# Optimization experiments

Hardware: AMD Instinct MI355X
Metric: run time of the kernel (lower is better)

The kernel has to match this reference:

```python
import jax, jax.numpy as jnp
import numpy as np

N0, N1, N2 = 200_000, 100_000, 80_000
F = 32
K5, K3 = 125, 27
M1, M2, M3, M4 = 20_000, 20_000, 30_000, 20_000
EPS = 1e-5


def sparse_conv(feats, W, in_idx, out_idx, n_out):
    """Gather-GEMM-scatter sparse conv. feats:[Nin,Cin], W:[K,Cin,Cout],
    in_idx/out_idx:[K,M] kernel map. Returns [n_out, Cout]."""
    g = feats[in_idx]                                  # [K, M, Cin] gather
    contrib = jnp.einsum('kmc,kcd->kmd', g, W)         # per-offset GEMM
    cout = W.shape[-1]
    out = jnp.zeros((n_out, cout), feats.dtype)
    return out.at[out_idx.reshape(-1)].add(contrib.reshape(-1, cout))


def bn(x, g, b):
    m = x.mean(0)
    v = x.var(0)
    return (x - m) * jax.lax.rsqrt(v + EPS) * g + b


def setup_inputs():
    key = jax.random.key(0)
    ks = jax.random.split(key, 16)
    W_SCALE = 0.02
    inp = {
        'x_feats': jax.random.normal(ks[0], (N0, 1), jnp.float32),
        'w1a': jax.random.normal(ks[1], (K5, 1, F), jnp.float32) * W_SCALE,
        'w1b': jax.random.normal(ks[2], (K5, F, F), jnp.float32) * W_SCALE,
        'w1c': jax.random.normal(ks[3], (K5, F, F), jnp.float32) * W_SCALE,
        'w2': jax.random.normal(ks[4], (K3, F, 2 * F), jnp.float32) * W_SCALE,
        'w3a': jax.random.normal(ks[5], (K3, 2 * F, 4 * F), jnp.float32) * W_SCALE,
        'w3b': jax.random.normal(ks[6], (K3, 4 * F, 8 * F), jnp.float32) * W_SCALE,
        'bn1b_g': jnp.ones((F,), jnp.float32), 'bn1b_b': jnp.zeros((F,), jnp.float32),
        'bn1c_g': jnp.ones((F,), jnp.float32), 'bn1c_b': jnp.zeros((F,), jnp.float32),
        'bn3a_g': jnp.ones((4 * F,), jnp.float32), 'bn3a_b': jnp.zeros((4 * F,), jnp.float32),
        'bn3b_g': jnp.ones((8 * F,), jnp.float32), 'bn3b_b': jnp.zeros((8 * F,), jnp.float32),
        'km1a_in': jax.random.randint(ks[7], (K5, M1), 0, N0, jnp.int32),
        'km1a_out': jax.random.randint(ks[8], (K5, M1), 0, N1, jnp.int32),
        'km1b_in': jax.random.randint(ks[9], (K5, M2), 0, N1, jnp.int32),
        'km1b_out': jax.random.randint(ks[10], (K5, M2), 0, N1, jnp.int32),
        'km1c_in': jax.random.randint(ks[11], (K5, M2), 0, N1, jnp.int32),
        'km1c_out': jax.random.randint(ks[12], (K5, M2), 0, N1, jnp.int32),
        'km2_in': jax.random.randint(ks[13], (K3, M3), 0, N1, jnp.int32),
        'km2_out': jax.random.randint(ks[14], (K3, M3), 0, N2, jnp.int32),
        'km3a_in': jax.random.randint(jax.random.fold_in(key, 20), (K3, M4), 0, N2, jnp.int32),
        'km3a_out': jax.random.randint(jax.random.fold_in(key, 21), (K3, M4), 0, N2, jnp.int32),
        'km3b_in': jax.random.randint(jax.random.fold_in(key, 22), (K3, M4), 0, N2, jnp.int32),
        'km3b_out': jax.random.randint(jax.random.fold_in(key, 23), (K3, M4), 0, N2, jnp.int32),
        'n1': N1,
        'n2': N2,
    }
    return inp


def reference(x_feats, w1a, w1b, w1c, w2, w3a, w3b,
              bn1b_g, bn1b_b, bn1c_g, bn1c_b, bn3a_g, bn3a_b, bn3b_g, bn3b_b,
              km1a_in, km1a_out, km1b_in, km1b_out, km1c_in, km1c_out,
              km2_in, km2_out, km3a_in, km3a_out, km3b_in, km3b_out, n1, n2):
    # enc1: conv(1->F, k5, s2) + ReLU
    h = jax.nn.relu(sparse_conv(x_feats, w1a, km1a_in, km1a_out, n1))
    # conv(F->F, k5) + BN + ReLU
    h = jax.nn.relu(bn(sparse_conv(h, w1b, km1b_in, km1b_out, n1), bn1b_g, bn1b_b))
    # conv(F->F, k5) + BN + ReLU
    x_e1 = jax.nn.relu(bn(sparse_conv(h, w1c, km1c_in, km1c_out, n1), bn1c_g, bn1c_b))
    # conv2: conv(F->2F, k3) onto c_out coordinates (no activation)
    h2 = sparse_conv(x_e1, w2, km2_in, km2_out, n2)
    # enc2: conv(2F->4F, k3) + BN + ReLU
    h2 = jax.nn.relu(bn(sparse_conv(h2, w3a, km3a_in, km3a_out, n2), bn3a_g, bn3a_b))
    # conv(4F->8F, k3) + BN + ReLU
    x_e2 = jax.nn.relu(bn(sparse_conv(h2, w3b, km3b_in, km3b_out, n2), bn3b_g, bn3b_b))
    return (x_e1, x_e2)
```

## Files before the change

kernel.cpp:

```cpp
#include <hip/hip_runtime.h>
#include <hip/hip_fp16.h>
#include <cstdint>
#include <algorithm>

#define N1c 100000
#define N2c 80000
#define EPSc 1e-5f
#define STRIDE_N1 102400
#define STRIDE_N2 81920

typedef _Float16 fp16x8 __attribute__((ext_vector_type(8)));
typedef float f32x4 __attribute__((ext_vector_type(4)));

__global__ __launch_bounds__(256) void rank2d_kernel(
    const int* __restrict__ out_idx, int* __restrict__ rank,
    int* __restrict__ bins, int E, int M, int q, int stride)
{
    for (int e = blockIdx.x * 256 + threadIdx.x; e < E; e += gridDim.x * 256) {
        int chunk = (e / M) / q;
        rank[e] = atomicAdd(&bins[chunk * stride + out_idx[e]], 1);
    }
}

__global__ __launch_bounds__(256) void scan1(
    const int* __restrict__ bins, int* __restrict__ ptr,
    int* __restrict__ bsums, int n)
{
    __shared__ int lds[256];
    int base = blockIdx.x * 1024;
    int v[4]; int t = 0;
    #pragma unroll
    for (int i = 0; i < 4; ++i) {
        int idx = base + threadIdx.x * 4 + i;
        v[i] = idx < n ? bins[idx] : 0;
        t += v[i];
    }
    lds[threadIdx.x] = t; __syncthreads();
    for (int off = 1; off < 256; off <<= 1) {
        int x = threadIdx.x >= off ? lds[threadIdx.x - off] : 0;
        __syncthreads();
        lds[threadIdx.x] += x;
        __syncthreads();
    }
    int run = lds[threadIdx.x] - t;
    if (threadIdx.x == 255) bsums[blockIdx.x] = lds[255];
    #pragma unroll
    for (int i = 0; i < 4; ++i) {
        int idx = base + threadIdx.x * 4 + i;
        if (idx < n) ptr[idx] = run;
        run += v[i];
    }
}

__global__ __launch_bounds__(64) void scan2s(
    int* __restrict__ bsums, int bpc, int nch)
{
    int c = threadIdx.x;
    if (c < nch) {
        int run = 0;
        for (int i = 0; i < bpc; ++i) {
            int idx = c * bpc + i;
            int t = bsums[idx]; bsums[idx] = run; run += t;
        }
    }
}

__global__ __launch_bounds__(256) void scan3(
    int* __restrict__ ptr, const int* __restrict__ bsums, int n)
{
    int idx = blockIdx.x * 1024 + threadIdx.x * 4;
    int add = bsums[blockIdx.x];
    #pragma unroll
    for (int i = 0; i < 4; ++i)
        if (idx + i < n) ptr[idx + i] += add;
}

__global__ __launch_bounds__(256) void wconv_fp16(
    const float* __restrict__ W, _Float16* __restrict__ Wh,
    int K, int CIN, int CTILE, int WST, int total)
{
    for (int idx = blockIdx.x * 256 + threadIdx.x; idx < total;
         idx += gridDim.x * 256) {
        int k = idx / (CTILE * CIN);
        int c = (idx / CIN) % CTILE;
        int j = idx % CIN;
        Wh[idx] = (_Float16)W[(size_t)k * CIN * WST + (size_t)j * WST + c];
    }
}

__global__ __launch_bounds__(256) void scatter_1a(
    const float* __restrict__ x, const int* __restrict__ iin,
    const int* __restrict__ iout, const int* __restrict__ ptr,
    const int* __restrict__ rank, float2* __restrict__ payload, int E, int M)
{
    for (int e = blockIdx.x * 256 + threadIdx.x; e < E; e += gridDim.x * 256) {
        int k = e / M;
        float2 p; p.x = x[iin[e]]; p.y = __int_as_float(k);
        payload[ptr[iout[e]] + rank[e]] = p;
    }
}

__global__ __launch_bounds__(256) void phaseB_1a(
    const float2* __restrict__ payload, const int* __restrict__ ptr,
    const float* __restrict__ W, __half* __restrict__ out, int n)
{
    __shared__ float Wl[125 * 32];
    for (int i = threadIdx.x; i < 125 * 32; i += 256) Wl[i] = W[i];
    __syncthreads();
    int total = n * 32;
    for (int idx = blockIdx.x * 256 + threadIdx.x; idx < total; idx += gridDim.x * 256) {
        int o = idx >> 5, c = idx & 31;
        int s0 = ptr[o], s1 = ptr[o + 1];
        float acc = 0.f;
        for (int s = s0; s < s1; ++s) {
            float2 p = payload[s];
            acc = fmaf(p.x, Wl[(__float_as_int(p.y) << 5) + c], acc);
        }
        out[idx] = __float2half(fmaxf(acc, 0.f));
    }
}

template <int CIN, int CTILE, int GMODE, int IN16>
__global__ __launch_bounds__(256, 3) void phaseA_mfma(
    const void* __restrict__ feats_, const _Float16* __restrict__ Wh,
    const int* __restrict__ in_idx, const int* __restrict__ out_idx,
    const int* __restrict__ ptr, const int* __restrict__ rank,
    __half* __restrict__ contrib, int M,
    const float* __restrict__ sc, const float* __restrict__ sh)
{
    constexpr int PP  = 64;
    constexpr int NK  = CIN / 32;
    constexpr int NCF = CTILE / 16;
    constexpr int GCHK = CIN / 8;
    constexpr int GSM  = (GCHK < 16 ? GCHK : 16) - 1;
    constexpr int RCH  = GCHK / 4;
    static_assert(CIN % 32 == 0 && CTILE % 16 == 0 && RCH >= 1, "");

    __shared__ __align__(16) _Float16 Gl[PP * CIN];
    __shared__ __align__(16) _Float16 Wt[CTILE * CIN];
    __shared__ int sslot[PP];

    const int tid  = threadIdx.x;
    const int wave = tid >> 6;
    const int lane = tid & 63;
    const int k    = blockIdx.y;

    const int* iin  = in_idx  + (size_t)k * M;
    const int* iout = out_idx + (size_t)k * M;
    const int* rk   = rank    + (size_t)k * M;
    const _Float16* Wk = Wh + (size_t)k * CTILE * CIN;

    for (int i = tid; i < CTILE * GCHK; i += 256) {
        int row = i / GCHK, ch = i % GCHK;
        fp16x8 v = *(const fp16x8*)&Wk[(size_t)row * CIN + ch * 8];
        *(fp16x8*)&Wt[row * CIN + ((ch ^ (row & GSM)) << 3)] = v;
    }

    for (int base = blockIdx.x * PP; base < M; base += gridDim.x * PP) {
        if (tid < PP && base + tid < M)
            sslot[tid] = ptr[iout[base + tid]] + rk[base + tid];

        {
            int r = tid & 63;
            int h = tid >> 6;
            int p = base + r;
            if (p < M) {
                const int c0 = h * (CIN / 4);
                if (IN16) {
                    const _Float16* fr =
                        (const _Float16*)feats_ + (size_t)iin[p] * CIN + c0;
                    #pragma unroll
                    for (int cc = 0; cc < RCH; ++cc) {
                        int c = cc * 8;
                        fp16x8 v = *(const fp16x8*)(fr + c);
                        if (GMODE == 2) {
                            #pragma unroll
                            for (int j = 0; j < 8; ++j) {
                                float x = fmaf((float)v[j], sc[c0 + c + j],
                                               sh[c0 + c + j]);
                                v[j] = (_Float16)fmaxf(x, 0.f);
                            }
                        }
                        int ch = (c0 + c) >> 3;
                        *(fp16x8*)&Gl[r * CIN + ((ch ^ (r & GSM)) << 3)] = v;
                    }
                } else {
                    const float* fr =
                        (const float*)feats_ + (size_t)iin[p] * CIN + c0;
                    #pragma unroll
                    for (int cc = 0; cc < RCH; ++cc) {
                        int c = cc * 8;
                        float a[8];
                        *(float4*)&a[0] = *(const float4*)(fr + c);
                        *(float4*)&a[4] = *(const float4*)(fr + c + 4);
                        if (GMODE == 2) {
                            #pragma unroll
                            for (int j = 0; j < 8; ++j)
                                a[j] = fmaxf(fmaf(a[j], sc[c0 + c + j],
                                                  sh[c0 + c + j]), 0.f);
                        }
                        fp16x8 v;
                        #pragma unroll
                        for (int j = 0; j < 8; ++j) v[j] = (_Float16)a[j];
                        int ch = (c0 + c) >> 3;
                        *(fp16x8*)&Gl[r * CIN + ((ch ^ (r & GSM)) << 3)] = v;
                    }
                }
            }
        }
        __syncthreads();

        f32x4 acc[NCF];
        #pragma unroll
        for (int cf = 0; cf < NCF; ++cf)
            acc[cf] = (f32x4){0.f, 0.f, 0.f, 0.f};

        const int lrow = lane & 15;
        const int lk8  = (lane >> 4) * 8;
        #pragma unroll
        for (int kk = 0; kk < NK; ++kk) {
            int col = kk * 32 + lk8;
            int r = wave * 16 + lrow;
            fp16x8 afr = *(const fp16x8*)
                &Gl[r * CIN + ((((col >> 3) ^ (r & GSM))) << 3)];
            #pragma unroll
            for (int cf = 0; cf < NCF; ++cf) {
                int rw = cf * 16 + lrow;
                fp16x8 bfr = *(const fp16x8*)
                    &Wt[rw * CIN + ((((col >> 3) ^ (rw & GSM))) << 3)];
                acc[cf] = __builtin_amdgcn_mfma_f32_16x16x32_f16(
                    afr, bfr, acc[cf], 0, 0, 0);
            }
        }

        {
            int prb = wave * 16 + (lane >> 4) * 4;
            #pragma unroll
            for (int b = 0; b < 4; ++b) {
                int pr = prb + b;
                if (base + pr < M) {
                    size_t s = (size_t)sslot[pr];
                    #pragma unroll
                    for (int cf = 0; cf < NCF; ++cf)
                        contrib[s * CTILE + cf * 16 + lrow] =
                            __float2half(acc[cf][b]);
                }
            }
        }
        __syncthreads();
    }
}

template <int CSTR, bool STATS, int OUT16>
__global__ __launch_bounds__(256) void phaseB8(
    const __half* __restrict__ contrib, const int* __restrict__ ptr,
    void* __restrict__ out_, int n, int ostr, int accum,
    double* __restrict__ statsbuf, int sqoff)
{
    float s1 = 0.f, s2 = 0.f;
    int total = n * CSTR;
    for (int idx = blockIdx.x * 256 + threadIdx.x; idx < total; idx += gridDim.x * 256) {
        int o = idx / CSTR, c = idx % CSTR;
        int a = ptr[o], b = ptr[o + 1];
        size_t oi = (size_t)o * ostr + c;
        float acc;
        if (OUT16)
            acc = accum ? __half2float(((const __half*)out_)[oi]) : 0.f;
        else
            acc = accum ? ((const float*)out_)[oi] : 0.f;
        for (int s = a; s < b; ++s)
            acc += __half2float(contrib[(size_t)s * CSTR + c]);
        if (OUT16) ((__half*)out_)[oi] = __float2half(acc);
        else       ((float*)out_)[oi] = acc;
        if (STATS) { s1 += acc; s2 += acc * acc; }
    }
    if constexpr (STATS) {
        __shared__ double l1[256], l2[256];
        l1[threadIdx.x] = (double)s1; l2[threadIdx.x] = (double)s2;
        __syncthreads();
        for (int off = 128; off >= CSTR; off >>= 1) {
            if (threadIdx.x < (unsigned)off) {
                l1[threadIdx.x] += l1[threadIdx.x + off];
                l2[threadIdx.x] += l2[threadIdx.x + off];
            }
            __syncthreads();
        }
        if (threadIdx.x < CSTR) {
            atomicAdd(&statsbuf[threadIdx.x], l1[threadIdx.x]);
            atomicAdd(&statsbuf[sqoff + threadIdx.x], l2[threadIdx.x]);
        }
    }
}

template <int C>
__global__ __launch_bounds__(256) void make_scsh(
    const double* __restrict__ sums, const float* __restrict__ g,
    const float* __restrict__ b, float* __restrict__ sc, float* __restrict__ sh,
    double inv_n)
{
    int c = threadIdx.x;
    if (c < C) {
        double mean = sums[c] * inv_n;
        double var  = sums[C + c] * inv_n - mean * mean;
        float s = g[c] * (float)(1.0 / sqrt(var + (double)EPSc));
        sc[c] = s;
        sh[c] = b[c] - (float)mean * s;
    }
}

template <int C>
__global__ __launch_bounds__(256) void bn_apply_relu_kernel(
    float* __restrict__ x, int n, const double* __restrict__ sums,
    const float* __restrict__ g, const float* __restrict__ b)
{
    const int c = threadIdx.x % C;
    const double inv_n = 1.0 / (double)n;
    double mean = sums[c] * inv_n;
    double var  = sums[C + c] * inv_n - mean * mean;
    float scale = g[c] * (float)(1.0 / sqrt(var + (double)EPSc));
    float shift = b[c] - (float)mean * scale;
    size_t total = (size_t)n * C;
    size_t stride = (size_t)gridDim.x * 256;
    for (size_t i = (size_t)blockIdx.x * 256 + threadIdx.x; i < total; i += stride)
        x[i] = fmaxf(x[i] * scale + shift, 0.f);
}

struct Plan { int q, nch; };

static Plan make_plan(long long tot_elems, int K, long long cap, int maxch)
{
    if (cap < 1) cap = 1;
    long long nch0 = (tot_elems + cap - 1) / cap;
    if (nch0 < 1) nch0 = 1;
    if (nch0 > K) nch0 = K;
    int q = (int)((K + nch0 - 1) / nch0);
    int nch = (K + q - 1) / q;
    if (nch > maxch) { q = (K + maxch - 1) / maxch; nch = (K + q - 1) / q; }
    return { q, nch };
}

static void build_csr2d(const int* iout, int* rank, int* bins, int* ptr, int* bsums,
                        int E, int M, int q, int nch, int stride, hipStream_t s)
{
    hipMemsetAsync(bins, 0, (size_t)nch * stride * sizeof(int), s);
    int gb = std::min(2048, (E + 255) / 256);
    hipLaunchKernelGGL(rank2d_kernel, dim3(gb), dim3(256), 0, s, iout, rank, bins, E, M, q, stride);
    int totalbins = nch * stride, nb = totalbins / 1024, bpc = stride / 1024;
    hipLaunchKernelGGL(scan1, dim3(nb), dim3(256), 0, s, bins, ptr, bsums, totalbins);
    hipLaunchKernelGGL(scan2s, dim3(1), dim3(64), 0, s, bsums, bpc, nch);
    hipLaunchKernelGGL(scan3, dim3(nb), dim3(256), 0, s, ptr, bsums, totalbins);
}

template <int CIN, int COUT, int GMODE, bool STATS, int IN16, int OUT16>
static void run_layer(const void* feats, const float* W,
                      const int* iin, const int* iout, void* outp,
                      int M, int K, int n_out, int stride, int maxch,
                      int* bins, int* ptr, int* bsums, int* rank, __half* contrib,
                      _Float16* wh, long long cap_f32,
                      const float* sc, const float* sh,
                      double* statsbuf, hipStream_t s)
{
    int wtot = K * COUT * CIN;
    hipLaunchKernelGGL(wconv_fp16, dim3(std::min(2048, (wtot + 255) / 256)),
                       dim3(256), 0, s, W, wh, K, CIN, COUT, COUT, wtot);
    long long cap_h = cap_f32 * 2;
    Plan pl = make_plan((long long)K * M * COUT, K, cap_h, maxch);
    build_csr2d(iout, rank, bins, ptr, bsums, K * M, M, pl.q, pl.nch, stride, s);
    for (int ch = 0; ch < pl.nch; ++ch) {
        int k0 = ch * pl.q;
        int qc = std::min(pl.q, K - k0);
        dim3 g((M + 63) / 64, qc);
        hipLaunchKernelGGL((phaseA_mfma<CIN, COUT, GMODE, IN16>), g, dim3(256), 0, s,
                           feats, wh + (size_t)k0 * COUT * CIN,
                           iin + (size_t)k0 * M, iout + (size_t)k0 * M,
                           ptr + (size_t)ch * stride, rank + (size_t)k0 * M,
                           contrib, M, sc, sh);
        bool last = (ch == pl.nch - 1);
        if (STATS && last)
            hipLaunchKernelGGL((phaseB8<COUT, true, OUT16>), dim3(2048), dim3(256), 0, s,
                               contrib, ptr + (size_t)ch * stride, outp, n_out, COUT,
                               ch ? 1 : 0, statsbuf, COUT);
        else
            hipLaunchKernelGGL((phaseB8<COUT, false, OUT16>), dim3(2048), dim3(256), 0, s,
                               contrib, ptr + (size_t)ch * stride, outp, n_out, COUT,
                               ch ? 1 : 0, (double*)nullptr, 0);
    }
}

extern "C" void kernel_launch(void* const* d_in, const int* in_sizes, int n_in,
                              void* d_out, int out_size, void* d_ws, size_t ws_size,
                              hipStream_t stream)
{
    const float* x_feats = (const float*)d_in[0];
    const float* w1a = (const float*)d_in[1];
    const float* w1b = (const float*)d_in[2];
    const float* w1c = (const float*)d_in[3];
    const float* w2  = (const float*)d_in[4];
    const float* w3a = (const float*)d_in[5];
    const float* w3b = (const float*)d_in[6];
    const float* bn1b_g = (const float*)d_in[7];
    const float* bn1b_b = (const float*)d_in[8];
    const float* bn1c_g = (const float*)d_in[9];
    const float* bn1c_b = (const float*)d_in[10];
    const float* bn3a_g = (const float*)d_in[11];
    const float* bn3a_b = (const float*)d_in[12];
    const float* bn3b_g = (const float*)d_in[13];
    const float* bn3b_b = (const float*)d_in[14];
    const int* km1a_in  = (const int*)d_in[15];
    const int* km1a_out = (const int*)d_in[16];
    const int* km1b_in  = (const int*)d_in[17];
    const int* km1b_out = (const int*)d_in[18];
    const int* km1c_in  = (const int*)d_in[19];
    const int* km1c_out = (const int*)d_in[20];
    const int* km2_in   = (const int*)d_in[21];
    const int* km2_out  = (const int*)d_in[22];
    const int* km3a_in  = (const int*)d_in[23];
    const int* km3a_out = (const int*)d_in[24];
    const int* km3b_in  = (const int*)d_in[25];
    const int* km3b_out = (const int*)d_in[26];

    float* out  = (float*)d_out;
    float* x_e1 = out;
    float* x_e2 = out + (size_t)N1c * 32;

    float* ws = (float*)d_ws;
    float*  poolA  = ws;
    float*  poolB  = poolA + 10240000;
    double* dstats = (double*)(poolB + 5120000);
    float*  scsh   = (float*)(dstats + 2048);
    int*    bins   = (int*)(scsh + 1024);
    int*    ptr    = bins + 819200;
    int*    bsums  = ptr + 819200;
    int*    rank   = bsums + 1024;
    float*  whf    = (float*)(rank + 2500000);
    _Float16* wh   = (_Float16*)whf;
    float*  contribf = whf + 221200;
    __half* contrib  = (__half*)contribf;
    const long long FIXED = 10240000LL + 5120000 + 4096 + 1024
                          + 819200 + 819200 + 1024 + 2500000 + 221200;
    long long cap = (long long)(ws_size / 4) - FIXED - 32;
    if (cap < 1) cap = 1;

    __half* h1  = (__half*)poolA;
    __half* h3  = (__half*)poolA;
    __half* h2  = (__half*)poolB;
    __half* h2b = (__half*)poolB;

    double* dst1b = dstats;
    double* dst1c = dstats + 512;
    double* dst3a = dstats + 1024;
    double* dst3b = dstats + 1536;
    float* sc1b = scsh,       *sh1b = scsh + 32;
    float* sc3a = scsh + 256, *sh3a = scsh + 384;

    hipMemsetAsync(dstats, 0, 2048 * sizeof(double), stream);

    {
        build_csr2d(km1a_out, rank, bins, ptr, bsums, 125 * 20000, 20000, 125, 1,
                    STRIDE_N1, stream);
        hipLaunchKernelGGL(scatter_1a, dim3(2048), dim3(256), 0, stream,
                           x_feats, km1a_in, km1a_out, ptr, rank, (float2*)contribf,
                           125 * 20000, 20000);
        hipLaunchKernelGGL(phaseB_1a, dim3(2048), dim3(256), 0, stream,
                           (const float2*)contribf, ptr, w1a, h1, N1c);
    }

    run_layer<32, 32, 0, true, 1, 1>(h1, w1b, km1b_in, km1b_out, h2, 20000, 125, N1c,
                                     STRIDE_N1, 8, bins, ptr, bsums, rank, contrib,
                                     wh, cap, nullptr, nullptr, dst1b, stream);
    hipLaunchKernelGGL((make_scsh<32>), dim3(1), dim3(256), 0, stream,
                       dst1b, bn1b_g, bn1b_b, sc1b, sh1b, 1.0 / N1c);

    run_layer<32, 32, 2, true, 1, 0>(h2, w1c, km1c_in, km1c_out, x_e1, 20000, 125, N1c,
                                     STRIDE_N1, 8, bins, ptr, bsums, rank, contrib,
                                     wh, cap, sc1b, sh1b, dst1c, stream);
    hipLaunchKernelGGL((bn_apply_relu_kernel<32>), dim3(2048), dim3(256), 0, stream,
                       x_e1, N1c, dst1c, bn1c_g, bn1c_b);

    run_layer<32, 64, 0, false, 0, 1>(x_e1, w2, km2_in, km2_out, h2b, 30000, 27, N2c,
                                      STRIDE_N2, 10, bins, ptr, bsums, rank, contrib,
                                      wh, cap, nullptr, nullptr, nullptr, stream);

    run_layer<64, 128, 0, true, 1, 1>(h2b, w3a, km3a_in, km3a_out, h3, 20000, 27, N2c,
                                      STRIDE_N2, 10, bins, ptr, bsums, rank, contrib,
                                      wh, cap, nullptr, nullptr, dst3a, stream);
    hipLaunchKernelGGL((make_scsh<128>), dim3(1), dim3(256), 0, stream,
                       dst3a, bn3a_g, bn3a_b, sc3a, sh3a, 1.0 / N2c);

    {
        const int M = 20000, K = 27;
        Plan pl = make_plan((long long)K * M * 128, K, cap * 2, 10);
        build_csr2d(km3b_out, rank, bins, ptr, bsums, K * M, M, pl.q, pl.nch,
                    STRIDE_N2, stream);
        for (int half = 0; half < 2; ++half) {
            int wtot = K * 128 * 128;
            hipLaunchKernelGGL(wconv_fp16, dim3(2048), dim3(256), 0, stream,
                               w3b + half * 128, wh, K, 128, 128, 256, wtot);
            for (int ch = 0; ch < pl.nch; ++ch) {
                int k0 = ch * pl.q;
                int qc = std::min(pl.q, K - k0);
                dim3 g((20000 + 63) / 64, qc);
                hipLaunchKernelGGL((phaseA_mfma<128, 128, 2, 1>), g, dim3(256), 0, stream,
                                   h3, wh + (size_t)k0 * 128 * 128,
                                   km3b_in + (size_t)k0 * M, km3b_out + (size_t)k0 * M,
                                   ptr + (size_t)ch * STRIDE_N2, rank + (size_t)k0 * M,
                                   contrib, M, sc3a, sh3a);
                bool last = (ch == pl.nch - 1);
                if (last)
                    hipLaunchKernelGGL((phaseB8<128, true, 0>), dim3(2048), dim3(256), 0, stream,
                                       contrib, ptr + (size_t)ch * STRIDE_N2,
                                       x_e2 + half * 128, N2c, 256, ch ? 1 : 0,
                                       dst3b + half * 128, 256);
                else
                    hipLaunchKernelGGL((phaseB8<128, false, 0>), dim3(2048), dim3(256), 0, stream,
                                       contrib, ptr + (size_t)ch * STRIDE_N2,
                                       x_e2 + half * 128, N2c, 256, ch ? 1 : 0,
                                       (double*)nullptr, 0);
            }
        }
        hipLaunchKernelGGL((bn_apply_relu_kernel<256>), dim3(2048), dim3(256), 0, stream,
                           x_e2, N2c, dst3b, bn3b_g, bn3b_b);
    }
}
```

Measured before the change: 1.898 ms.

## Compute all 256 output channels of last conv in one pass; fp16 shadow for conv2 input

The final 128->256 sparse conv used to run twice, once per 128-channel half, which repeated the gather, the CSR chunk loop and the scatter-reduce passes. A new MFMA kernel gathers each input row once and loops over both weight halves in shared memory, writing 256-wide fp16 contributions that a single phaseB pass reduces. This removes the duplicate gather and reduction work but doubles the contribution buffer per chunk, which can mean more chunks and a larger LDS footprint. Separately, the BN-apply for x_e1 now also writes an fp16 copy, so conv2 gathers half-width features instead of fp32.

Result: faster. 1.841 ms (-3.0%).

```diff
diff --git a/kernel.cpp b/kernel.cpp
--- a/kernel.cpp
+++ b/kernel.cpp
@@ -251,6 +251,113 @@
     }
 }
 
+template <int GMODE>
+__global__ __launch_bounds__(256, 3) void phaseA_mfma_3b(
+    const void* __restrict__ feats_, const _Float16* __restrict__ Wh,
+    const int* __restrict__ in_idx, const int* __restrict__ out_idx,
+    const int* __restrict__ ptr, const int* __restrict__ rank,
+    __half* __restrict__ contrib, int M,
+    const float* __restrict__ sc, const float* __restrict__ sh)
+{
+    constexpr int CIN = 128, PP = 64, NK = 4, NCF = 8;
+    constexpr int GCHK = 16, GSM = 15, RCH = 4;
+
+    __shared__ __align__(16) _Float16 Gl[PP * CIN];
+    __shared__ __align__(16) _Float16 Wt[128 * CIN];
+    __shared__ int sslot[PP];
+
+    const int tid  = threadIdx.x;
+    const int wave = tid >> 6;
+    const int lane = tid & 63;
+    const int k    = blockIdx.y;
+
+    const _Float16* feats = (const _Float16*)feats_;
+    const int* iin  = in_idx  + (size_t)k * M;
+    const int* iout = out_idx + (size_t)k * M;
+    const int* rk   = rank    + (size_t)k * M;
+    const _Float16* Wk = Wh + (size_t)k * 256 * CIN;
+
+    const int lrow = lane & 15;
+    const int lk8  = (lane >> 4) * 8;
+
+    for (int base = blockIdx.x * PP; base < M; base += gridDim.x * PP) {
+        if (tid < PP && base + tid < M)
+            sslot[tid] = ptr[iout[base + tid]] + rk[base + tid];
+
+        {
+            int r = tid & 63;
+            int h = tid >> 6;
+            int p = base + r;
+            if (p < M) {
+                const int c0 = h * 32;
+                const _Float16* fr = feats + (size_t)iin[p] * CIN + c0;
+                #pragma unroll
+                for (int cc = 0; cc < RCH; ++cc) {
+                    int c = cc * 8;
+                    fp16x8 v = *(const fp16x8*)(fr + c);
+                    if (GMODE == 2) {
+                        #pragma unroll
+                        for (int j = 0; j < 8; ++j) {
+                            float x = fmaf((float)v[j], sc[c0 + c + j],
+                                           sh[c0 + c + j]);
+                            v[j] = (_Float16)fmaxf(x, 0.f);
+                        }
+                    }
+                    int ch = (c0 + c) >> 3;
+                    *(fp16x8*)&Gl[r * CIN + ((ch ^ (r & GSM)) << 3)] = v;
+                }
+            }
+        }
+
+        #pragma unroll
+        for (int half = 0; half < 2; ++half) {
+            __syncthreads();
+            for (int i = tid; i < 128 * GCHK; i += 256) {
+                int row = i / GCHK, ch = i % GCHK;
+                fp16x8 v = *(const fp16x8*)
+                    &Wk[(size_t)(half * 128 + row) * CIN + ch * 8];
+                *(fp16x8*)&Wt[row * CIN + ((ch ^ (row & GSM)) << 3)] = v;
+            }
+            __syncthreads();
+
+            f32x4 acc[NCF];
+            #pragma unroll
+            for (int cf = 0; cf < NCF; ++cf)
+                acc[cf] = (f32x4){0.f, 0.f, 0.f, 0.f};
+
+            #pragma unroll
+            for (int kk = 0; kk < NK; ++kk) {
+                int col = kk * 32 + lk8;
+                int r = wave * 16 + lrow;
+                fp16x8 afr = *(const fp16x8*)
+                    &Gl[r * CIN + ((((col >> 3) ^ (r & GSM))) << 3)];
+                #pragma unroll
+                for (int cf = 0; cf < NCF; ++cf) {
+                    int rw = cf * 16 + lrow;
+                    fp16x8 bfr = *(const fp16x8*)
+                        &Wt[rw * CIN + ((((col >> 3) ^ (rw & GSM))) << 3)];
+                    acc[cf] = __builtin_amdgcn_mfma_f32_16x16x32_f16(
+                        afr, bfr, acc[cf], 0, 0, 0);
+                }
+            }
+
+            int prb = wave * 16 + (lane >> 4) * 4;
+            #pragma unroll
+            for (int b = 0; b < 4; ++b) {
+                int pr = prb + b;
+                if (base + pr < M) {
+                    size_t s = (size_t)sslot[pr];
+                    #pragma unroll
+                    for (int cf = 0; cf < NCF; ++cf)
+                        contrib[s * 256 + half * 128 + cf * 16 + lrow] =
+                            __float2half(acc[cf][b]);
+                }
+            }
+        }
+        __syncthreads();
+    }
+}
+
 template <int CSTR, bool STATS, int OUT16>
 __global__ __launch_bounds__(256) void phaseB8(
     const __half* __restrict__ contrib, const int* __restrict__ ptr,
@@ -323,6 +430,27 @@
     size_t stride = (size_t)gridDim.x * 256;
     for (size_t i = (size_t)blockIdx.x * 256 + threadIdx.x; i < total; i += stride)
         x[i] = fmaxf(x[i] * scale + shift, 0.f);
+}
+
+template <int C>
+__global__ __launch_bounds__(256) void bn_apply_relu_shadow_kernel(
+    float* __restrict__ x, __half* __restrict__ xh, int n,
+    const double* __restrict__ sums,
+    const float* __restrict__ g, const float* __restrict__ b)
+{
+    const int c = threadIdx.x % C;
+    const double inv_n = 1.0 / (double)n;
+    double mean = sums[c] * inv_n;
+    double var  = sums[C + c] * inv_n - mean * mean;
+    float scale = g[c] * (float)(1.0 / sqrt(var + (double)EPSc));
+    float shift = b[c] - (float)mean * scale;
+    size_t total = (size_t)n * C;
+    size_t stride = (size_t)gridDim.x * 256;
+    for (size_t i = (size_t)blockIdx.x * 256 + threadIdx.x; i < total; i += stride) {
+        float v = fmaxf(x[i] * scale + shift, 0.f);
+        x[i] = v;
+        xh[i] = __float2half(v);
+    }
 }
 
 struct Plan { int q, nch; };
@@ -434,10 +562,10 @@
     int*    rank   = bsums + 1024;
     float*  whf    = (float*)(rank + 2500000);
     _Float16* wh   = (_Float16*)whf;
-    float*  contribf = whf + 221200;
+    float*  contribf = whf + 442400;
     __half* contrib  = (__half*)contribf;
     const long long FIXED = 10240000LL + 5120000 + 4096 + 1024
-                          + 819200 + 819200 + 1024 + 2500000 + 221200;
+                          + 819200 + 819200 + 1024 + 2500000 + 442400;
     long long cap = (long long)(ws_size / 4) - FIXED - 32;
     if (cap < 1) cap = 1;
 
@@ -445,6 +573,7 @@
     __half* h3  = (__half*)poolA;
     __half* h2  = (__half*)poolB;
     __half* h2b = (__half*)poolB;
+    __half* xe1h = (__half*)poolB + 5120000;
 
     double* dst1b = dstats;
     double* dst1c = dstats + 512;
@@ -474,10 +603,10 @@
     run_layer<32, 32, 2, true, 1, 0>(h2, w1c, km1c_in, km1c_out, x_e1, 20000, 125, N1c,
                                      STRIDE_N1, 8, bins, ptr, bsums, rank, contrib,
                                      wh, cap, sc1b, sh1b, dst1c, stream);
-    hipLaunchKernelGGL((bn_apply_relu_kernel<32>), dim3(2048), dim3(256), 0, stream,
-                       x_e1, N1c, dst1c, bn1c_g, bn1c_b);
-
-    run_layer<32, 64, 0, false, 0, 1>(x_e1, w2, km2_in, km2_out, h2b, 30000, 27, N2c,
+    hipLaunchKernelGGL((bn_apply_relu_shadow_kernel<32>), dim3(2048), dim3(256), 0, stream,
+                       x_e1, xe1h, N1c, dst1c, bn1c_g, bn1c_b);
+
+    run_layer<32, 64, 0, false, 1, 1>(xe1h, w2, km2_in, km2_out, h2b, 30000, 27, N2c,
                                       STRIDE_N2, 10, bins, ptr, bsums, rank, contrib,
                                       wh, cap, nullptr, nullptr, nullptr, stream);
 
@@ -489,34 +618,30 @@
 
     {
         const int M = 20000, K = 27;
-        Plan pl = make_plan((long long)K * M * 128, K, cap * 2, 10);
+        int wtot = K * 256 * 128;
+        hipLaunchKernelGGL(wconv_fp16, dim3(2048), dim3(256), 0, stream,
+                           w3b, wh, K, 128, 256, 256, wtot);
+        Plan pl = make_plan((long long)K * M * 256, K, cap * 2, 10);
         build_csr2d(km3b_out, rank, bins, ptr, bsums, K * M, M, pl.q, pl.nch,
                     STRIDE_N2, stream);
-        for (int half = 0; half < 2; ++half) {
-            int wtot = K * 128 * 128;
-            hipLaunchKernelGGL(wconv_fp16, dim3(2048), dim3(256), 0, stream,
-                               w3b + half * 128, wh, K, 128, 128, 256, wtot);
-            for (int ch = 0; ch < pl.nch; ++ch) {
-                int k0 = ch * pl.q;
-                int qc = std::min(pl.q, K - k0);
-                dim3 g((20000 + 63) / 64, qc);
-                hipLaunchKernelGGL((phaseA_mfma<128, 128, 2, 1>), g, dim3(256), 0, stream,
-                                   h3, wh + (size_t)k0 * 128 * 128,
-                                   km3b_in + (size_t)k0 * M, km3b_out + (size_t)k0 * M,
-                                   ptr + (size_t)ch * STRIDE_N2, rank + (size_t)k0 * M,
-                                   contrib, M, sc3a, sh3a);
-                bool last = (ch == pl.nch - 1);
-                if (last)
-                    hipLaunchKernelGGL((phaseB8<128, true, 0>), dim3(2048), dim3(256), 0, stream,
-                                       contrib, ptr + (size_t)ch * STRIDE_N2,
-                                       x_e2 + half * 128, N2c, 256, ch ? 1 : 0,
-                                       dst3b + half * 128, 256);
-                else
-                    hipLaunchKernelGGL((phaseB8<128, false, 0>), dim3(2048), dim3(256), 0, stream,
-                                       contrib, ptr + (size_t)ch * STRIDE_N2,
-                                       x_e2 + half * 128, N2c, 256, ch ? 1 : 0,
-                                       (double*)nullptr, 0);
-            }
+        for (int ch = 0; ch < pl.nch; ++ch) {
+            int k0 = ch * pl.q;
+            int qc = std::min(pl.q, K - k0);
+            dim3 g((M + 63) / 64, qc);
+            hipLaunchKernelGGL((phaseA_mfma_3b<2>), g, dim3(256), 0, stream,
+                               (const void*)h3, wh + (size_t)k0 * 256 * 128,
+                               km3b_in + (size_t)k0 * M, km3b_out + (size_t)k0 * M,
+                               ptr + (size_t)ch * STRIDE_N2, rank + (size_t)k0 * M,
+                               contrib, M, sc3a, sh3a);
+            bool last = (ch == pl.nch - 1);
+            if (last)
+                hipLaunchKernelGGL((phaseB8<256, true, 0>), dim3(2048), dim3(256), 0, stream,
+                                   contrib, ptr + (size_t)ch * STRIDE_N2,
+                                   x_e2, N2c, 256, ch ? 1 : 0, dst3b, 256);
+            else
+                hipLaunchKernelGGL((phaseB8<256, false, 0>), dim3(2048), dim3(256), 0, stream,
+                                   contrib, ptr + (size_t)ch * STRIDE_N2,
+                                   x_e2, N2c, 256, ch ? 1 : 0, (double*)nullptr, 0);
         }
         hipLaunchKernelGGL((bn_apply_relu_kernel<256>), dim3(2048), dim3(256), 0, stream,
                            x_e2, N2c, dst3b, bn3b_g, bn3b_b);
```
